# Kernel tuning notes

Measured on AMD Instinct MI355X. Metric: run time of the kernel, lower is better.

Reference implementation:

```python
import jax, jax.numpy as jnp
import numpy as np

B, S, D, T = 8, 4096, 512, 8  # batch, seq (dim), d_model, nheads


def _sinusoidal_pe(dim, d_model):
    # matches torch: pe[:,0::2]=sin(pos*div), pe[:,1::2]=cos(pos*div)
    pos = jnp.arange(dim, dtype=jnp.float32)[:, None]
    div = jnp.exp(jnp.arange(0, d_model, 2, dtype=jnp.float32) * (-(np.log(10000.0) / d_model)))
    ang = pos * div  # [dim, d_model//2]
    return jnp.stack([jnp.sin(ang), jnp.cos(ang)], axis=-1).reshape(dim, d_model)


def setup_inputs() -> dict:
    key = jax.random.key(0)
    ks = jax.random.split(key, 7)
    sc = 1.0 / np.sqrt(D)
    return {
        "x": jax.random.normal(ks[0], (B, S, D), dtype=jnp.float32),
        "Wk": jax.random.normal(ks[1], (T, D, D), dtype=jnp.float32) * sc,
        "bk": jax.random.normal(ks[2], (T, D), dtype=jnp.float32) * sc,
        "Wq": jax.random.normal(ks[3], (T, D, D), dtype=jnp.float32) * sc,
        "bq": jax.random.normal(ks[4], (T, D), dtype=jnp.float32) * sc,
        "Wv": jax.random.normal(ks[5], (T, D, D), dtype=jnp.float32) * sc,
        "bv": jax.random.normal(ks[6], (T, D), dtype=jnp.float32) * sc,
    }


def reference(x, Wk, bk, Wq, bq, Wv, bv):
    b, s, d = x.shape
    t = Wk.shape[0]
    c = s // t  # head chunk length
    x = x + _sinusoidal_pe(s, d)[None]  # PE add
    xh = x.reshape(b, t, c, d)  # 'b (t c) d -> b t c d'
    # torch Linear: y = x @ W^T + b ; W is [out, in]
    k = jnp.einsum('btcd,ted->btce', xh, Wk) + bk[None, :, None, :]
    q = jnp.einsum('btcd,ted->btce', xh, Wq) + bq[None, :, None, :]
    v = jnp.einsum('btcd,ted->btce', xh, Wv) + bv[None, :, None, :]
    # note: k @ q^T (not q @ k^T) and divide by d_model (not sqrt) -- faithful
    scores = jnp.einsum('btid,btjd->btij', k, q) * (1.0 / d)
    attn = jax.nn.softmax(scores, axis=-1)
    out = jnp.einsum('btij,btjd->btid', attn, v)
    return out.reshape(b, s, d)  # concat heads along seq dim
```

## Files before the change

kernel.cpp:

```cpp
#include <hip/hip_runtime.h>
#include <hip/hip_bf16.h>
#include <cstdint>
#include <cstddef>


typedef __bf16 bf16_t;
typedef __bf16 bf16x4 __attribute__((ext_vector_type(4)));
typedef __bf16 bf16x8 __attribute__((ext_vector_type(8)));
typedef float  f32x4  __attribute__((ext_vector_type(4)));

#define GAS __attribute__((address_space(1)))
#define LAS __attribute__((address_space(3)))

__global__ __launch_bounds__(256) void pe_cast_kernel(
    const float* __restrict__ x, bf16_t* __restrict__ xpe)
{
    const float cexp = -0.017988946039015984f;
    int i = blockIdx.x * 256 + threadIdx.x;
    int d4 = i & 127;
    int s  = i >> 7;
    int d  = d4 * 4;
    float fs = (float)s;
    float a0 = fs * __expf(cexp * (float)d);
    float a1 = fs * __expf(cexp * (float)(d + 2));
    float s0, c0, s1, c1;
    sincosf(a0, &s0, &c0);
    sincosf(a1, &s1, &c1);
    size_t base = (size_t)s * 512 + d;
    #pragma unroll
    for (int b = 0; b < 8; ++b) {
        float4 xv = *(const float4*)(x + (size_t)b * 2097152 + base);
        bf16x4 o;
        o[0] = (bf16_t)(xv.x + s0);
        o[1] = (bf16_t)(xv.y + c0);
        o[2] = (bf16_t)(xv.z + s1);
        o[3] = (bf16_t)(xv.w + c1);
        *(bf16x4*)(xpe + (size_t)b * 2097152 + base) = o;
    }
}

__global__ __launch_bounds__(256) void cast_w(
    const float* __restrict__ w0, const float* __restrict__ w1, const float* __restrict__ w2,
    bf16_t* __restrict__ o0, bf16_t* __restrict__ o1, bf16_t* __restrict__ o2, int n4)
{
    const float* s = blockIdx.y == 0 ? w0 : (blockIdx.y == 1 ? w1 : w2);
    bf16_t*      o = blockIdx.y == 0 ? o0 : (blockIdx.y == 1 ? o1 : o2);
    for (int i = blockIdx.x * 256 + threadIdx.x; i < n4; i += gridDim.x * 256) {
        float4 v = ((const float4*)s)[i];
        bf16x4 r;
        r[0] = (bf16_t)v.x; r[1] = (bf16_t)v.y; r[2] = (bf16_t)v.z; r[3] = (bf16_t)v.w;
        ((bf16x4*)o)[i] = r;
    }
}

template<int BIAS_MODE, int OUT_BF16>
__global__ __launch_bounds__(256, 2) void gemm_nt(
    const bf16_t* __restrict__ A, const bf16_t* __restrict__ Bm,
    void* __restrict__ C, const float* __restrict__ bias,
    long aStr, long bStr, long cStr, int aByT, int bByT, float scale)
{
    constexpr int LD = 512;
    int L  = blockIdx.y * 16 + blockIdx.x;
    int wk = (L & 7) * 128 + (L >> 3);
    int bt = wk >> 4;
    int tile = wk & 15;
    int t  = bt & 7;
    const bf16_t* Ab = A  + (size_t)(aByT ? t : bt) * aStr;
    const bf16_t* Bb = Bm + (size_t)(bByT ? t : bt) * bStr;
    int ti = (tile >> 2) << 7;
    int tn = (tile & 3) << 7;

    __shared__ __align__(1024) char lds[65536];

    const int tid  = threadIdx.x;
    const int l    = tid & 63;
    const int w    = tid >> 6;
    const int lrow = l >> 3;
    const int hd   = (l & 7) ^ lrow;
    const int wrow = w >> 1, wcol = w & 1;
    const int rA   = l & 15;
    const int hb   = l >> 4;
    const int x7   = l & 7;

    f32x4 acc[4][4] = {};

    auto stage = [&](int buf, int k0) {
        char* ldsA = lds + buf * 32768;
        char* ldsB = ldsA + 16384;
        #pragma unroll
        for (int p = 0; p < 4; ++p) {
            int c    = w * 4 + p;
            int grow = c * 8 + lrow;
            const bf16_t* srcA = Ab + (size_t)(ti + grow) * LD + k0 + hd * 8;
            const bf16_t* srcB = Bb + (size_t)(tn + grow) * LD + k0 + hd * 8;
            __builtin_amdgcn_global_load_lds((GAS void*)srcA, (LAS void*)(ldsA + c * 1024 + l * 16), 16, 0, 0);
            __builtin_amdgcn_global_load_lds((GAS void*)srcB, (LAS void*)(ldsB + c * 1024 + l * 16), 16, 0, 0);
        }
    };

    stage(0, 0);
    __syncthreads();
    for (int it = 0; it < 8; ++it) {
        if (it < 7) stage((it + 1) & 1, (it + 1) * 64);
        const char* ldsA = lds + (it & 1) * 32768;
        const char* ldsB = ldsA + 16384;
        #pragma unroll
        for (int kk = 0; kk < 2; ++kk) {
            bf16x8 a[4], b[4];
            #pragma unroll
            for (int m = 0; m < 4; ++m) {
                int off = (wrow * 64 + m * 16 + rA) * 128 + ((((kk << 2) | hb)) ^ x7) * 16;
                a[m] = *(const bf16x8*)(ldsA + off);
            }
            #pragma unroll
            for (int n = 0; n < 4; ++n) {
                int off = (wcol * 64 + n * 16 + rA) * 128 + ((((kk << 2) | hb)) ^ x7) * 16;
                b[n] = *(const bf16x8*)(ldsB + off);
            }
            #pragma unroll
            for (int m = 0; m < 4; ++m)
                #pragma unroll
                for (int n = 0; n < 4; ++n)
                    acc[m][n] = __builtin_amdgcn_mfma_f32_16x16x32_bf16(a[m], b[n], acc[m][n], 0, 0, 0);
        }
        __syncthreads();
    }

    const float* biasT = bias ? bias + t * 512 : bias;
    int r0 = ti + wrow * 64;
    int c0 = tn + wcol * 64;
    #pragma unroll
    for (int m = 0; m < 4; ++m) {
        #pragma unroll
        for (int n = 0; n < 4; ++n) {
            int col = c0 + n * 16 + rA;
            float bc = (BIAS_MODE == 1) ? biasT[col] : 0.0f;
            f32x4 v = acc[m][n];
            #pragma unroll
            for (int r = 0; r < 4; ++r) {
                int row = r0 + m * 16 + hb * 4 + r;
                float val = v[r] * scale + ((BIAS_MODE == 2) ? biasT[row] : bc);
                size_t off = (size_t)bt * cStr + (size_t)row * LD + col;
                if (OUT_BF16) ((bf16_t*)C)[off] = (bf16_t)val;
                else          ((float*)C)[off]  = val;
            }
        }
    }
}

__global__ __launch_bounds__(512, 2) void scores_softmax(
    const bf16_t* __restrict__ K, const bf16_t* __restrict__ Q,
    bf16_t* __restrict__ P)
{
    int L  = blockIdx.x;
    int wk = (L & 7) * 32 + (L >> 3);
    int bt = wk >> 2;
    int ti = (wk & 3) << 7;
    const bf16_t* Kb = K + (size_t)bt * 262144;
    const bf16_t* Qb = Q + (size_t)bt * 262144;

    __shared__ __align__(1024) char smem[86016];
    float* smax_p = (float*)(smem + 81920);
    float* ssum_p = (float*)(smem + 83968);

    const int tid  = threadIdx.x;
    const int l    = tid & 63;
    const int wv   = tid >> 6;
    const int wrow = wv >> 2;
    const int wcol = wv & 3;
    const int rA   = l & 15;
    const int hb   = l >> 4;

    f32x4 acc[4][8] = {};

    auto stage = [&](int buf, int d0) {
        char* kA = smem + buf * 8192;
        char* qB = smem + 16384 + buf * 32768;
        {
            int row = tid >> 2, slot = tid & 3;
            const bf16_t* src = Kb + (size_t)(ti + row) * 512 + d0 + (slot ^ (row & 3)) * 8;
            __builtin_amdgcn_global_load_lds((GAS void*)src, (LAS void*)(kA + tid * 16), 16, 0, 0);
        }
        #pragma unroll
        for (int u = 0; u < 4; ++u) {
            int q2 = u * 512 + tid;
            int row = q2 >> 2, slot = q2 & 3;
            const bf16_t* src = Qb + (size_t)row * 512 + d0 + (slot ^ (row & 3)) * 8;
            __builtin_amdgcn_global_load_lds((GAS void*)src, (LAS void*)(qB + q2 * 16), 16, 0, 0);
        }
    };

    stage(0, 0);
    __syncthreads();
    for (int it = 0; it < 16; ++it) {
        if (it < 15) stage((it + 1) & 1, (it + 1) * 32);
        const char* kA = smem + (it & 1) * 8192;
        const char* qB = smem + 16384 + (it & 1) * 32768;
        bf16x8 a[4], b[8];
        #pragma unroll
        for (int m = 0; m < 4; ++m) {
            int row = wrow * 64 + m * 16 + rA;
            a[m] = *(const bf16x8*)(kA + row * 64 + (hb ^ (row & 3)) * 16);
        }
        #pragma unroll
        for (int n = 0; n < 8; ++n) {
            int row = wcol * 128 + n * 16 + rA;
            b[n] = *(const bf16x8*)(qB + row * 64 + (hb ^ (row & 3)) * 16);
        }
        #pragma unroll
        for (int m = 0; m < 4; ++m)
            #pragma unroll
            for (int n = 0; n < 8; ++n)
                acc[m][n] = __builtin_amdgcn_mfma_f32_16x16x32_bf16(a[m], b[n], acc[m][n], 0, 0, 0);
        __syncthreads();
    }

    float red[4][4];
    #pragma unroll
    for (int m = 0; m < 4; ++m)
        #pragma unroll
        for (int r = 0; r < 4; ++r) {
            float mx = acc[m][0][r];
            #pragma unroll
            for (int n = 1; n < 8; ++n) mx = fmaxf(mx, acc[m][n][r]);
            #pragma unroll
            for (int o = 1; o < 16; o <<= 1) mx = fmaxf(mx, __shfl_xor(mx, o, 64));
            red[m][r] = mx;
        }
    if (rA < 4) {
        #pragma unroll
        for (int m = 0; m < 4; ++m)
            smax_p[(wrow * 64 + m * 16 + hb * 4 + rA) * 4 + wcol] = red[m][rA];
    }
    __syncthreads();
    float rstat[4][4];
    #pragma unroll
    for (int m = 0; m < 4; ++m)
        #pragma unroll
        for (int r = 0; r < 4; ++r) {
            f32x4 p4 = *(const f32x4*)(smax_p + (wrow * 64 + m * 16 + hb * 4 + r) * 4);
            rstat[m][r] = fmaxf(fmaxf(p4[0], p4[1]), fmaxf(p4[2], p4[3]));
        }
    const float inv512 = 1.0f / 512.0f;
    #pragma unroll
    for (int m = 0; m < 4; ++m)
        #pragma unroll
        for (int r = 0; r < 4; ++r) {
            float sum = 0.0f;
            #pragma unroll
            for (int n = 0; n < 8; ++n) {
                float e = __expf((acc[m][n][r] - rstat[m][r]) * inv512);
                acc[m][n][r] = e;
                sum += e;
            }
            #pragma unroll
            for (int o = 1; o < 16; o <<= 1) sum += __shfl_xor(sum, o, 64);
            red[m][r] = sum;
        }
    if (rA < 4) {
        #pragma unroll
        for (int m = 0; m < 4; ++m)
            ssum_p[(wrow * 64 + m * 16 + hb * 4 + rA) * 4 + wcol] = red[m][rA];
    }
    __syncthreads();
    #pragma unroll
    for (int m = 0; m < 4; ++m)
        #pragma unroll
        for (int r = 0; r < 4; ++r) {
            f32x4 p4 = *(const f32x4*)(ssum_p + (wrow * 64 + m * 16 + hb * 4 + r) * 4);
            rstat[m][r] = 1.0f / (((p4[0] + p4[1]) + (p4[2] + p4[3])));
        }
    #pragma unroll
    for (int m = 0; m < 4; ++m)
        #pragma unroll
        for (int n = 0; n < 8; ++n) {
            int col = wcol * 128 + n * 16 + rA;
            #pragma unroll
            for (int r = 0; r < 4; ++r) {
                int row = ti + wrow * 64 + m * 16 + hb * 4 + r;
                P[(size_t)bt * 262144 + (size_t)row * 512 + col] =
                    (bf16_t)(acc[m][n][r] * rstat[m][r]);
            }
        }
}

extern "C" void kernel_launch(void* const* d_in, const int* in_sizes, int n_in,
                              void* d_out, int out_size, void* d_ws, size_t ws_size,
                              hipStream_t stream)
{
    const float* x  = (const float*)d_in[0];
    const float* Wk = (const float*)d_in[1];
    const float* bk = (const float*)d_in[2];
    const float* Wq = (const float*)d_in[3];
    const float* bq = (const float*)d_in[4];
    const float* Wv = (const float*)d_in[5];
    const float* bv = (const float*)d_in[6];
    float* out = (float*)d_out;
    char*  ws  = (char*)d_ws;

    bf16_t* k    = (bf16_t*)(ws + 0);
    bf16_t* q    = (bf16_t*)(ws + 33554432);
    bf16_t* vt   = (bf16_t*)(ws + 67108864);
    bf16_t* xpe  = (bf16_t*)(ws + 100663296);
    bf16_t* attn = xpe;
    bf16_t* wkb  = (bf16_t*)(ws + 134217728);
    bf16_t* wqb  = (bf16_t*)(ws + 138412032);
    bf16_t* wvb  = (bf16_t*)(ws + 142606336);

    const long S2 = 262144;

    pe_cast_kernel<<<2048, 256, 0, stream>>>(x, xpe);
    cast_w<<<dim3(512, 3), 256, 0, stream>>>(Wk, Wq, Wv, wkb, wqb, wvb, (8 * 512 * 512) / 4);

    dim3 gg(16, 64);
    gemm_nt<1, 1><<<gg, 256, 0, stream>>>(xpe, wkb, k, bk, S2, S2, S2, 0, 1, 1.0f);
    gemm_nt<1, 1><<<gg, 256, 0, stream>>>(xpe, wqb, q, bq, S2, S2, S2, 0, 1, 1.0f);
    gemm_nt<2, 1><<<gg, 256, 0, stream>>>(wvb, xpe, vt, bv, S2, S2, S2, 1, 0, 1.0f);
    scores_softmax<<<256, 512, 0, stream>>>(k, q, attn);
    gemm_nt<0, 0><<<gg, 256, 0, stream>>>(attn, vt, out, nullptr, S2, S2, S2, 0, 0, 1.0f);
}
```

Before: 274.1 us.

## Fuse K/Q projections into one GEMM and fuse softmax with PV product

Adds a gemm_kq kernel that computes the K and Q projections together, sharing one staged tile of the PE-added input and reading both weight sets straight from global memory. The softmax kernel becomes attn_fused: it writes the normalized probabilities into swizzled LDS and multiplies them by V^T in the same block, so the bf16 attention matrix never goes to global memory and one launch is removed. The cost is more LDS per block (about 132 KB), which likely limits occupancy to one block per CU. B operands in both new kernels are loaded uncoalesced from global memory without LDS staging, which may hurt bandwidth.

```diff
diff --git a/kernel.cpp b/kernel.cpp
--- a/kernel.cpp
+++ b/kernel.cpp
@@ -53,6 +53,99 @@
     }
 }
 
+__global__ __launch_bounds__(256, 2) void gemm_kq(
+    const bf16_t* __restrict__ X, const bf16_t* __restrict__ WK,
+    const bf16_t* __restrict__ WQ, bf16_t* __restrict__ Ko,
+    bf16_t* __restrict__ Qo, const float* __restrict__ bk,
+    const float* __restrict__ bq)
+{
+    int L  = blockIdx.y * 16 + blockIdx.x;
+    int wk = (L & 7) * 128 + (L >> 3);
+    int bt = wk >> 4;
+    int tile = wk & 15;
+    int t  = bt & 7;
+    const bf16_t* Ab = X  + (size_t)bt * 262144;
+    const bf16_t* Kw = WK + (size_t)t * 262144;
+    const bf16_t* Qw = WQ + (size_t)t * 262144;
+    int ti = (tile >> 2) << 7;
+    int tn = (tile & 3) << 7;
+
+    __shared__ __align__(1024) char lds[32768];
+
+    const int tid  = threadIdx.x;
+    const int l    = tid & 63;
+    const int w    = tid >> 6;
+    const int lrow = l >> 3;
+    const int hd   = (l & 7) ^ lrow;
+    const int wrow = w >> 1, wcol = w & 1;
+    const int rA   = l & 15;
+    const int hb   = l >> 4;
+    const int x7   = l & 7;
+
+    f32x4 acck[4][4] = {}, accq[4][4] = {};
+
+    auto stage = [&](int buf, int k0) {
+        char* ldsA = lds + buf * 16384;
+        #pragma unroll
+        for (int p = 0; p < 4; ++p) {
+            int c    = w * 4 + p;
+            int grow = c * 8 + lrow;
+            const bf16_t* srcA = Ab + (size_t)(ti + grow) * 512 + k0 + hd * 8;
+            __builtin_amdgcn_global_load_lds((GAS void*)srcA, (LAS void*)(ldsA + c * 1024 + l * 16), 16, 0, 0);
+        }
+    };
+
+    stage(0, 0);
+    __syncthreads();
+    for (int it = 0; it < 8; ++it) {
+        if (it < 7) stage((it + 1) & 1, (it + 1) * 64);
+        const char* ldsA = lds + (it & 1) * 16384;
+        #pragma unroll
+        for (int kk = 0; kk < 2; ++kk) {
+            bf16x8 a[4], bK[4], bQ[4];
+            #pragma unroll
+            for (int m = 0; m < 4; ++m) {
+                int off = (wrow * 64 + m * 16 + rA) * 128 + (((kk << 2) | hb) ^ x7) * 16;
+                a[m] = *(const bf16x8*)(ldsA + off);
+            }
+            int kpos = it * 64 + kk * 32 + hb * 8;
+            #pragma unroll
+            for (int n = 0; n < 4; ++n) {
+                int e = tn + wcol * 64 + n * 16 + rA;
+                bK[n] = *(const bf16x8*)(Kw + (size_t)e * 512 + kpos);
+                bQ[n] = *(const bf16x8*)(Qw + (size_t)e * 512 + kpos);
+            }
+            #pragma unroll
+            for (int m = 0; m < 4; ++m)
+                #pragma unroll
+                for (int n = 0; n < 4; ++n) {
+                    acck[m][n] = __builtin_amdgcn_mfma_f32_16x16x32_bf16(a[m], bK[n], acck[m][n], 0, 0, 0);
+                    accq[m][n] = __builtin_amdgcn_mfma_f32_16x16x32_bf16(a[m], bQ[n], accq[m][n], 0, 0, 0);
+                }
+        }
+        __syncthreads();
+    }
+
+    const float* bkT = bk + t * 512;
+    const float* bqT = bq + t * 512;
+    int r0 = ti + wrow * 64;
+    int c0 = tn + wcol * 64;
+    #pragma unroll
+    for (int m = 0; m < 4; ++m)
+        #pragma unroll
+        for (int n = 0; n < 4; ++n) {
+            int col = c0 + n * 16 + rA;
+            float bkc = bkT[col], bqc = bqT[col];
+            #pragma unroll
+            for (int r = 0; r < 4; ++r) {
+                int row = r0 + m * 16 + hb * 4 + r;
+                size_t off = (size_t)bt * 262144 + (size_t)row * 512 + col;
+                Ko[off] = (bf16_t)(acck[m][n][r] + bkc);
+                Qo[off] = (bf16_t)(accq[m][n][r] + bqc);
+            }
+        }
+}
+
 template<int BIAS_MODE, int OUT_BF16>
 __global__ __launch_bounds__(256, 2) void gemm_nt(
     const bf16_t* __restrict__ A, const bf16_t* __restrict__ Bm,
@@ -109,12 +202,12 @@
             bf16x8 a[4], b[4];
             #pragma unroll
             for (int m = 0; m < 4; ++m) {
-                int off = (wrow * 64 + m * 16 + rA) * 128 + ((((kk << 2) | hb)) ^ x7) * 16;
+                int off = (wrow * 64 + m * 16 + rA) * 128 + (((kk << 2) | hb) ^ x7) * 16;
                 a[m] = *(const bf16x8*)(ldsA + off);
             }
             #pragma unroll
             for (int n = 0; n < 4; ++n) {
-                int off = (wcol * 64 + n * 16 + rA) * 128 + ((((kk << 2) | hb)) ^ x7) * 16;
+                int off = (wcol * 64 + n * 16 + rA) * 128 + (((kk << 2) | hb) ^ x7) * 16;
                 b[n] = *(const bf16x8*)(ldsB + off);
             }
             #pragma unroll
@@ -130,7 +223,7 @@
     int r0 = ti + wrow * 64;
     int c0 = tn + wcol * 64;
     #pragma unroll
-    for (int m = 0; m < 4; ++m) {
+    for (int m = 0; m < 4; ++m)
         #pragma unroll
         for (int n = 0; n < 4; ++n) {
             int col = c0 + n * 16 + rA;
@@ -145,23 +238,23 @@
                 else          ((float*)C)[off]  = val;
             }
         }
-    }
-}
-
-__global__ __launch_bounds__(512, 2) void scores_softmax(
+}
+
+__global__ __launch_bounds__(512, 2) void attn_fused(
     const bf16_t* __restrict__ K, const bf16_t* __restrict__ Q,
-    bf16_t* __restrict__ P)
+    const bf16_t* __restrict__ VT, float* __restrict__ Out)
 {
     int L  = blockIdx.x;
-    int wk = (L & 7) * 32 + (L >> 3);
-    int bt = wk >> 2;
-    int ti = (wk & 3) << 7;
-    const bf16_t* Kb = K + (size_t)bt * 262144;
-    const bf16_t* Qb = Q + (size_t)bt * 262144;
-
-    __shared__ __align__(1024) char smem[86016];
-    float* smax_p = (float*)(smem + 81920);
-    float* ssum_p = (float*)(smem + 83968);
+    int wkd = (L & 7) * 32 + (L >> 3);
+    int bt = wkd >> 2;
+    int ti = (wkd & 3) << 7;
+    const bf16_t* Kb = K  + (size_t)bt * 262144;
+    const bf16_t* Qb = Q  + (size_t)bt * 262144;
+    const bf16_t* Vb = VT + (size_t)bt * 262144;
+
+    __shared__ __align__(1024) char smem[135168];
+    float* smax_p = (float*)(smem + 131072);
+    float* ssum_p = (float*)(smem + 133120);
 
     const int tid  = threadIdx.x;
     const int l    = tid & 63;
@@ -268,18 +361,54 @@
         #pragma unroll
         for (int r = 0; r < 4; ++r) {
             f32x4 p4 = *(const f32x4*)(ssum_p + (wrow * 64 + m * 16 + hb * 4 + r) * 4);
-            rstat[m][r] = 1.0f / (((p4[0] + p4[1]) + (p4[2] + p4[3])));
-        }
+            rstat[m][r] = 1.0f / ((p4[0] + p4[1]) + (p4[2] + p4[3]));
+        }
+
     #pragma unroll
     for (int m = 0; m < 4; ++m)
         #pragma unroll
         for (int n = 0; n < 8; ++n) {
-            int col = wcol * 128 + n * 16 + rA;
+            int j = wcol * 128 + n * 16 + rA;
+            int jslot = j >> 3, jrem = (j & 7) * 2;
             #pragma unroll
             for (int r = 0; r < 4; ++r) {
-                int row = ti + wrow * 64 + m * 16 + hb * 4 + r;
-                P[(size_t)bt * 262144 + (size_t)row * 512 + col] =
+                int i = wrow * 64 + m * 16 + hb * 4 + r;
+                *(bf16_t*)(smem + i * 1024 + ((jslot ^ (i & 7)) << 4) + jrem) =
                     (bf16_t)(acc[m][n][r] * rstat[m][r]);
+            }
+        }
+    __syncthreads();
+
+    f32x4 acc2[4][8] = {};
+    for (int it = 0; it < 16; ++it) {
+        int j0 = it * 32;
+        bf16x8 a[4], b[8];
+        #pragma unroll
+        for (int m = 0; m < 4; ++m) {
+            int i = wrow * 64 + m * 16 + rA;
+            a[m] = *(const bf16x8*)(smem + i * 1024 + ((((it << 2) | hb) ^ (i & 7)) << 4));
+        }
+        #pragma unroll
+        for (int n = 0; n < 8; ++n) {
+            int e = wcol * 128 + n * 16 + rA;
+            b[n] = *(const bf16x8*)(Vb + (size_t)e * 512 + j0 + hb * 8);
+        }
+        #pragma unroll
+        for (int m = 0; m < 4; ++m)
+            #pragma unroll
+            for (int n = 0; n < 8; ++n)
+                acc2[m][n] = __builtin_amdgcn_mfma_f32_16x16x32_bf16(a[m], b[n], acc2[m][n], 0, 0, 0);
+    }
+
+    #pragma unroll
+    for (int m = 0; m < 4; ++m)
+        #pragma unroll
+        for (int n = 0; n < 8; ++n) {
+            int e = wcol * 128 + n * 16 + rA;
+            #pragma unroll
+            for (int r = 0; r < 4; ++r) {
+                int i = ti + wrow * 64 + m * 16 + hb * 4 + r;
+                Out[(size_t)bt * 262144 + (size_t)i * 512 + e] = acc2[m][n][r];
             }
         }
 }
@@ -302,7 +431,6 @@
     bf16_t* q    = (bf16_t*)(ws + 33554432);
     bf16_t* vt   = (bf16_t*)(ws + 67108864);
     bf16_t* xpe  = (bf16_t*)(ws + 100663296);
-    bf16_t* attn = xpe;
     bf16_t* wkb  = (bf16_t*)(ws + 134217728);
     bf16_t* wqb  = (bf16_t*)(ws + 138412032);
     bf16_t* wvb  = (bf16_t*)(ws + 142606336);
@@ -313,9 +441,7 @@
     cast_w<<<dim3(512, 3), 256, 0, stream>>>(Wk, Wq, Wv, wkb, wqb, wvb, (8 * 512 * 512) / 4);
 
     dim3 gg(16, 64);
-    gemm_nt<1, 1><<<gg, 256, 0, stream>>>(xpe, wkb, k, bk, S2, S2, S2, 0, 1, 1.0f);
-    gemm_nt<1, 1><<<gg, 256, 0, stream>>>(xpe, wqb, q, bq, S2, S2, S2, 0, 1, 1.0f);
+    gemm_kq<<<gg, 256, 0, stream>>>(xpe, wkb, wqb, k, q, bk, bq);
     gemm_nt<2, 1><<<gg, 256, 0, stream>>>(wvb, xpe, vt, bv, S2, S2, S2, 1, 0, 1.0f);
-    scores_softmax<<<256, 512, 0, stream>>>(k, q, attn);
-    gemm_nt<0, 0><<<gg, 256, 0, stream>>>(attn, vt, out, nullptr, S2, S2, S2, 0, 0, 1.0f);
-}
+    attn_fused<<<256, 512, 0, stream>>>(k, q, vt, out);
+}
```

After: 327.3 us. +19.4%, slower.

## Fuse scores-softmax with PV matmul and merge prep kernels

Applied to the files above, without the earlier changes.

Replaces the separate scores/softmax kernel and the final P@V GEMM with a single attention kernel. Each block handles 64 query rows, keeps the normalized probabilities in swizzled LDS and streams V^T tiles to produce the fp32 output directly, so the bf16 attention matrix is never written to or re-read from global memory. The PE-add cast and the weight cast are merged into one launch, and the GEMM block-to-tile mapping is reordered to group heads. The fused kernel uses about 140KB of LDS, which limits it to one block per CU, and the K/Q tiles are smaller per block.

```diff
diff --git a/kernel.cpp b/kernel.cpp
--- a/kernel.cpp
+++ b/kernel.cpp
@@ -12,44 +12,48 @@
 #define GAS __attribute__((address_space(1)))
 #define LAS __attribute__((address_space(3)))
 
-__global__ __launch_bounds__(256) void pe_cast_kernel(
-    const float* __restrict__ x, bf16_t* __restrict__ xpe)
+__global__ __launch_bounds__(256) void prep_kernel(
+    const float* __restrict__ x, bf16_t* __restrict__ xpe,
+    const float* __restrict__ w0, const float* __restrict__ w1,
+    const float* __restrict__ w2, bf16_t* __restrict__ o0,
+    bf16_t* __restrict__ o1, bf16_t* __restrict__ o2)
 {
-    const float cexp = -0.017988946039015984f;
-    int i = blockIdx.x * 256 + threadIdx.x;
-    int d4 = i & 127;
-    int s  = i >> 7;
-    int d  = d4 * 4;
-    float fs = (float)s;
-    float a0 = fs * __expf(cexp * (float)d);
-    float a1 = fs * __expf(cexp * (float)(d + 2));
-    float s0, c0, s1, c1;
-    sincosf(a0, &s0, &c0);
-    sincosf(a1, &s1, &c1);
-    size_t base = (size_t)s * 512 + d;
-    #pragma unroll
-    for (int b = 0; b < 8; ++b) {
-        float4 xv = *(const float4*)(x + (size_t)b * 2097152 + base);
-        bf16x4 o;
-        o[0] = (bf16_t)(xv.x + s0);
-        o[1] = (bf16_t)(xv.y + c0);
-        o[2] = (bf16_t)(xv.z + s1);
-        o[3] = (bf16_t)(xv.w + c1);
-        *(bf16x4*)(xpe + (size_t)b * 2097152 + base) = o;
-    }
-}
-
-__global__ __launch_bounds__(256) void cast_w(
-    const float* __restrict__ w0, const float* __restrict__ w1, const float* __restrict__ w2,
-    bf16_t* __restrict__ o0, bf16_t* __restrict__ o1, bf16_t* __restrict__ o2, int n4)
-{
-    const float* s = blockIdx.y == 0 ? w0 : (blockIdx.y == 1 ? w1 : w2);
-    bf16_t*      o = blockIdx.y == 0 ? o0 : (blockIdx.y == 1 ? o1 : o2);
-    for (int i = blockIdx.x * 256 + threadIdx.x; i < n4; i += gridDim.x * 256) {
-        float4 v = ((const float4*)s)[i];
-        bf16x4 r;
-        r[0] = (bf16_t)v.x; r[1] = (bf16_t)v.y; r[2] = (bf16_t)v.z; r[3] = (bf16_t)v.w;
-        ((bf16x4*)o)[i] = r;
+    if (blockIdx.x < 2048) {
+        const float cexp = -0.017988946039015984f;
+        int i = blockIdx.x * 256 + threadIdx.x;
+        int d4 = i & 127;
+        int s  = i >> 7;
+        int d  = d4 * 4;
+        float fs = (float)s;
+        float a0 = fs * __expf(cexp * (float)d);
+        float a1 = fs * __expf(cexp * (float)(d + 2));
+        float s0, c0, s1, c1;
+        sincosf(a0, &s0, &c0);
+        sincosf(a1, &s1, &c1);
+        size_t base = (size_t)s * 512 + d;
+        #pragma unroll
+        for (int b = 0; b < 8; ++b) {
+            float4 xv = *(const float4*)(x + (size_t)b * 2097152 + base);
+            bf16x4 o;
+            o[0] = (bf16_t)(xv.x + s0);
+            o[1] = (bf16_t)(xv.y + c0);
+            o[2] = (bf16_t)(xv.z + s1);
+            o[3] = (bf16_t)(xv.w + c1);
+            *(bf16x4*)(xpe + (size_t)b * 2097152 + base) = o;
+        }
+    } else {
+        const int per = 524288;
+        for (int i = (blockIdx.x - 2048) * 256 + threadIdx.x; i < 3 * per;
+             i += 1024 * 256) {
+            int f = i / per, off = i - f * per;
+            const float* s = f == 0 ? w0 : (f == 1 ? w1 : w2);
+            bf16_t*      o = f == 0 ? o0 : (f == 1 ? o1 : o2);
+            float4 v = ((const float4*)s)[off];
+            bf16x4 r;
+            r[0] = (bf16_t)v.x; r[1] = (bf16_t)v.y;
+            r[2] = (bf16_t)v.z; r[3] = (bf16_t)v.w;
+            ((bf16x4*)o)[off] = r;
+        }
     }
 }
 
@@ -61,10 +65,10 @@
 {
     constexpr int LD = 512;
     int L  = blockIdx.y * 16 + blockIdx.x;
-    int wk = (L & 7) * 128 + (L >> 3);
-    int bt = wk >> 4;
-    int tile = wk & 15;
-    int t  = bt & 7;
+    int t  = L & 7;
+    int b  = (L >> 3) & 7;
+    int tile = L >> 6;
+    int bt = (b << 3) | t;
     const bf16_t* Ab = A  + (size_t)(aByT ? t : bt) * aStr;
     const bf16_t* Bb = Bm + (size_t)(bByT ? t : bt) * bStr;
     int ti = (tile >> 2) << 7;
@@ -106,22 +110,22 @@
         const char* ldsB = ldsA + 16384;
         #pragma unroll
         for (int kk = 0; kk < 2; ++kk) {
-            bf16x8 a[4], b[4];
+            bf16x8 a[4], bb[4];
             #pragma unroll
             for (int m = 0; m < 4; ++m) {
-                int off = (wrow * 64 + m * 16 + rA) * 128 + ((((kk << 2) | hb)) ^ x7) * 16;
+                int off = (wrow * 64 + m * 16 + rA) * 128 + (((kk << 2) | hb) ^ x7) * 16;
                 a[m] = *(const bf16x8*)(ldsA + off);
             }
             #pragma unroll
             for (int n = 0; n < 4; ++n) {
-                int off = (wcol * 64 + n * 16 + rA) * 128 + ((((kk << 2) | hb)) ^ x7) * 16;
-                b[n] = *(const bf16x8*)(ldsB + off);
+                int off = (wcol * 64 + n * 16 + rA) * 128 + (((kk << 2) | hb) ^ x7) * 16;
+                bb[n] = *(const bf16x8*)(ldsB + off);
             }
             #pragma unroll
             for (int m = 0; m < 4; ++m)
                 #pragma unroll
                 for (int n = 0; n < 4; ++n)
-                    acc[m][n] = __builtin_amdgcn_mfma_f32_16x16x32_bf16(a[m], b[n], acc[m][n], 0, 0, 0);
+                    acc[m][n] = __builtin_amdgcn_mfma_f32_16x16x32_bf16(a[m], bb[n], acc[m][n], 0, 0, 0);
         }
         __syncthreads();
     }
@@ -130,7 +134,7 @@
     int r0 = ti + wrow * 64;
     int c0 = tn + wcol * 64;
     #pragma unroll
-    for (int m = 0; m < 4; ++m) {
+    for (int m = 0; m < 4; ++m)
         #pragma unroll
         for (int n = 0; n < 4; ++n) {
             int col = c0 + n * 16 + rA;
@@ -145,72 +149,73 @@
                 else          ((float*)C)[off]  = val;
             }
         }
-    }
 }
 
-__global__ __launch_bounds__(512, 2) void scores_softmax(
+__global__ __launch_bounds__(512) void attn_fused(
     const bf16_t* __restrict__ K, const bf16_t* __restrict__ Q,
-    bf16_t* __restrict__ P)
+    const bf16_t* __restrict__ VT, float* __restrict__ Out)
 {
     int L  = blockIdx.x;
-    int wk = (L & 7) * 32 + (L >> 3);
-    int bt = wk >> 2;
-    int ti = (wk & 3) << 7;
-    const bf16_t* Kb = K + (size_t)bt * 262144;
-    const bf16_t* Qb = Q + (size_t)bt * 262144;
-
-    __shared__ __align__(1024) char smem[86016];
-    float* smax_p = (float*)(smem + 81920);
-    float* ssum_p = (float*)(smem + 83968);
-
-    const int tid  = threadIdx.x;
-    const int l    = tid & 63;
-    const int wv   = tid >> 6;
-    const int wrow = wv >> 2;
-    const int wcol = wv & 3;
-    const int rA   = l & 15;
-    const int hb   = l >> 4;
-
-    f32x4 acc[4][8] = {};
-
-    auto stage = [&](int buf, int d0) {
-        char* kA = smem + buf * 8192;
-        char* qB = smem + 16384 + buf * 32768;
-        {
-            int row = tid >> 2, slot = tid & 3;
-            const bf16_t* src = Kb + (size_t)(ti + row) * 512 + d0 + (slot ^ (row & 3)) * 8;
+    int bt = ((L >> 6) << 3) | (L & 7);
+    int ti = ((L >> 3) & 7) << 6;
+    const bf16_t* Kb = K  + (size_t)bt * 262144;
+    const bf16_t* Qb = Q  + (size_t)bt * 262144;
+    const bf16_t* Vb = VT + (size_t)bt * 262144;
+
+    __shared__ __align__(1024) char smem[143360];
+    char* Pl = smem + 73728;
+    float* smax_p = (float*)(smem + 139264);
+    float* ssum_p = (float*)(smem + 141312);
+
+    const int tid = threadIdx.x;
+    const int l   = tid & 63;
+    const int wv  = tid >> 6;
+    const int rA  = l & 15;
+    const int hb  = l >> 4;
+    const int key = (rA >> 1) & 3;
+
+    const int srow = tid >> 2;
+    const int sslot = tid & 3;
+
+    f32x4 acc[4][4] = {};
+
+    auto stageKQ = [&](int buf, int d0) {
+        char* kA = smem + buf * 4096;
+        char* qB = smem + 8192 + buf * 32768;
+        if (tid < 256) {
+            const bf16_t* src = Kb + (size_t)(ti + srow) * 512 + d0 +
+                                (sslot ^ ((srow >> 1) & 3)) * 8;
             __builtin_amdgcn_global_load_lds((GAS void*)src, (LAS void*)(kA + tid * 16), 16, 0, 0);
         }
         #pragma unroll
         for (int u = 0; u < 4; ++u) {
             int q2 = u * 512 + tid;
             int row = q2 >> 2, slot = q2 & 3;
-            const bf16_t* src = Qb + (size_t)row * 512 + d0 + (slot ^ (row & 3)) * 8;
+            const bf16_t* src = Qb + (size_t)row * 512 + d0 +
+                                (slot ^ ((row >> 1) & 3)) * 8;
             __builtin_amdgcn_global_load_lds((GAS void*)src, (LAS void*)(qB + q2 * 16), 16, 0, 0);
         }
     };
 
-    stage(0, 0);
+    stageKQ(0, 0);
     __syncthreads();
     for (int it = 0; it < 16; ++it) {
-        if (it < 15) stage((it + 1) & 1, (it + 1) * 32);
-        const char* kA = smem + (it & 1) * 8192;
-        const char* qB = smem + 16384 + (it & 1) * 32768;
-        bf16x8 a[4], b[8];
-        #pragma unroll
-        for (int m = 0; m < 4; ++m) {
-            int row = wrow * 64 + m * 16 + rA;
-            a[m] = *(const bf16x8*)(kA + row * 64 + (hb ^ (row & 3)) * 16);
-        }
-        #pragma unroll
-        for (int n = 0; n < 8; ++n) {
-            int row = wcol * 128 + n * 16 + rA;
-            b[n] = *(const bf16x8*)(qB + row * 64 + (hb ^ (row & 3)) * 16);
-        }
-        #pragma unroll
-        for (int m = 0; m < 4; ++m)
-            #pragma unroll
-            for (int n = 0; n < 8; ++n)
+        if (it < 15) stageKQ((it + 1) & 1, (it + 1) * 32);
+        const char* kA = smem + (it & 1) * 4096;
+        const char* qB = smem + 8192 + (it & 1) * 32768;
+        bf16x8 a[4], b[4];
+        #pragma unroll
+        for (int m = 0; m < 4; ++m)
+            a[m] = *(const bf16x8*)(kA + (m * 16 + rA) * 64 + ((hb ^ key) << 4));
+        #pragma unroll
+        for (int n = 0; n < 4; ++n) {
+            int j = wv * 64 + n * 16 + rA;
+            b[n] = *(const bf16x8*)(qB + j * 64 + ((hb ^ key) << 4));
+        }
+        #pragma unroll
+        for (int m = 0; m < 4; ++m)
+            #pragma unroll
+            for (int n = 0; n < 4; ++n)
                 acc[m][n] = __builtin_amdgcn_mfma_f32_16x16x32_bf16(a[m], b[n], acc[m][n], 0, 0, 0);
         __syncthreads();
     }
@@ -222,7 +227,7 @@
         for (int r = 0; r < 4; ++r) {
             float mx = acc[m][0][r];
             #pragma unroll
-            for (int n = 1; n < 8; ++n) mx = fmaxf(mx, acc[m][n][r]);
+            for (int n = 1; n < 4; ++n) mx = fmaxf(mx, acc[m][n][r]);
             #pragma unroll
             for (int o = 1; o < 16; o <<= 1) mx = fmaxf(mx, __shfl_xor(mx, o, 64));
             red[m][r] = mx;
@@ -230,7 +235,7 @@
     if (rA < 4) {
         #pragma unroll
         for (int m = 0; m < 4; ++m)
-            smax_p[(wrow * 64 + m * 16 + hb * 4 + rA) * 4 + wcol] = red[m][rA];
+            smax_p[(m * 16 + hb * 4 + rA) * 8 + wv] = red[m][rA];
     }
     __syncthreads();
     float rstat[4][4];
@@ -238,8 +243,11 @@
     for (int m = 0; m < 4; ++m)
         #pragma unroll
         for (int r = 0; r < 4; ++r) {
-            f32x4 p4 = *(const f32x4*)(smax_p + (wrow * 64 + m * 16 + hb * 4 + r) * 4);
-            rstat[m][r] = fmaxf(fmaxf(p4[0], p4[1]), fmaxf(p4[2], p4[3]));
+            int row = m * 16 + hb * 4 + r;
+            f32x4 p0 = *(const f32x4*)(smax_p + row * 8);
+            f32x4 p1 = *(const f32x4*)(smax_p + row * 8 + 4);
+            rstat[m][r] = fmaxf(fmaxf(fmaxf(p0[0], p0[1]), fmaxf(p0[2], p0[3])),
+                                fmaxf(fmaxf(p1[0], p1[1]), fmaxf(p1[2], p1[3])));
         }
     const float inv512 = 1.0f / 512.0f;
     #pragma unroll
@@ -248,7 +256,7 @@
         for (int r = 0; r < 4; ++r) {
             float sum = 0.0f;
             #pragma unroll
-            for (int n = 0; n < 8; ++n) {
+            for (int n = 0; n < 4; ++n) {
                 float e = __expf((acc[m][n][r] - rstat[m][r]) * inv512);
                 acc[m][n][r] = e;
                 sum += e;
@@ -260,26 +268,82 @@
     if (rA < 4) {
         #pragma unroll
         for (int m = 0; m < 4; ++m)
-            ssum_p[(wrow * 64 + m * 16 + hb * 4 + rA) * 4 + wcol] = red[m][rA];
+            ssum_p[(m * 16 + hb * 4 + rA) * 8 + wv] = red[m][rA];
     }
     __syncthreads();
     #pragma unroll
     for (int m = 0; m < 4; ++m)
         #pragma unroll
         for (int r = 0; r < 4; ++r) {
-            f32x4 p4 = *(const f32x4*)(ssum_p + (wrow * 64 + m * 16 + hb * 4 + r) * 4);
-            rstat[m][r] = 1.0f / (((p4[0] + p4[1]) + (p4[2] + p4[3])));
-        }
-    #pragma unroll
-    for (int m = 0; m < 4; ++m)
-        #pragma unroll
-        for (int n = 0; n < 8; ++n) {
-            int col = wcol * 128 + n * 16 + rA;
+            int row = m * 16 + hb * 4 + r;
+            f32x4 p0 = *(const f32x4*)(ssum_p + row * 8);
+            f32x4 p1 = *(const f32x4*)(ssum_p + row * 8 + 4);
+            rstat[m][r] = 1.0f / (((p0[0] + p0[1]) + (p0[2] + p0[3])) +
+                                  ((p1[0] + p1[1]) + (p1[2] + p1[3])));
+        }
+
+    #pragma unroll
+    for (int m = 0; m < 4; ++m)
+        #pragma unroll
+        for (int n = 0; n < 4; ++n) {
+            int j = wv * 64 + n * 16 + rA;
+            int jslot = j >> 3, jrem = (j & 7) * 2;
             #pragma unroll
             for (int r = 0; r < 4; ++r) {
-                int row = ti + wrow * 64 + m * 16 + hb * 4 + r;
-                P[(size_t)bt * 262144 + (size_t)row * 512 + col] =
+                int i = m * 16 + hb * 4 + r;
+                *(bf16_t*)(Pl + i * 1024 + ((jslot ^ (i & 7)) << 4) + jrem) =
                     (bf16_t)(acc[m][n][r] * rstat[m][r]);
+            }
+        }
+    __syncthreads();
+
+    auto stageV = [&](int buf, int j0) {
+        char* vB = smem + 8192 + buf * 32768;
+        #pragma unroll
+        for (int u = 0; u < 4; ++u) {
+            int q2 = u * 512 + tid;
+            int e = q2 >> 2, slot = q2 & 3;
+            const bf16_t* src = Vb + (size_t)e * 512 + j0 +
+                                (slot ^ ((e >> 1) & 3)) * 8;
+            __builtin_amdgcn_global_load_lds((GAS void*)src, (LAS void*)(vB + q2 * 16), 16, 0, 0);
+        }
+    };
+
+    f32x4 acc2[4][4] = {};
+    stageV(0, 0);
+    __syncthreads();
+    for (int it = 0; it < 16; ++it) {
+        if (it < 15) stageV((it + 1) & 1, (it + 1) * 32);
+        const char* vB = smem + 8192 + (it & 1) * 32768;
+        int jcb = it * 4;
+        bf16x8 a[4], b[4];
+        #pragma unroll
+        for (int m = 0; m < 4; ++m) {
+            int i = m * 16 + rA;
+            a[m] = *(const bf16x8*)(Pl + i * 1024 + (((jcb + hb) ^ (i & 7)) << 4));
+        }
+        #pragma unroll
+        for (int n = 0; n < 4; ++n) {
+            int e = wv * 64 + n * 16 + rA;
+            b[n] = *(const bf16x8*)(vB + e * 64 + ((hb ^ key) << 4));
+        }
+        #pragma unroll
+        for (int m = 0; m < 4; ++m)
+            #pragma unroll
+            for (int n = 0; n < 4; ++n)
+                acc2[m][n] = __builtin_amdgcn_mfma_f32_16x16x32_bf16(a[m], b[n], acc2[m][n], 0, 0, 0);
+        __syncthreads();
+    }
+
+    #pragma unroll
+    for (int m = 0; m < 4; ++m)
+        #pragma unroll
+        for (int n = 0; n < 4; ++n) {
+            int e = wv * 64 + n * 16 + rA;
+            #pragma unroll
+            for (int r = 0; r < 4; ++r) {
+                int i = ti + m * 16 + hb * 4 + r;
+                Out[(size_t)bt * 262144 + (size_t)i * 512 + e] = acc2[m][n][r];
             }
         }
 }
@@ -302,20 +366,17 @@
     bf16_t* q    = (bf16_t*)(ws + 33554432);
     bf16_t* vt   = (bf16_t*)(ws + 67108864);
     bf16_t* xpe  = (bf16_t*)(ws + 100663296);
-    bf16_t* attn = xpe;
     bf16_t* wkb  = (bf16_t*)(ws + 134217728);
     bf16_t* wqb  = (bf16_t*)(ws + 138412032);
     bf16_t* wvb  = (bf16_t*)(ws + 142606336);
 
     const long S2 = 262144;
 
-    pe_cast_kernel<<<2048, 256, 0, stream>>>(x, xpe);
-    cast_w<<<dim3(512, 3), 256, 0, stream>>>(Wk, Wq, Wv, wkb, wqb, wvb, (8 * 512 * 512) / 4);
+    prep_kernel<<<3072, 256, 0, stream>>>(x, xpe, Wk, Wq, Wv, wkb, wqb, wvb);
 
     dim3 gg(16, 64);
     gemm_nt<1, 1><<<gg, 256, 0, stream>>>(xpe, wkb, k, bk, S2, S2, S2, 0, 1, 1.0f);
     gemm_nt<1, 1><<<gg, 256, 0, stream>>>(xpe, wqb, q, bq, S2, S2, S2, 0, 1, 1.0f);
     gemm_nt<2, 1><<<gg, 256, 0, stream>>>(wvb, xpe, vt, bv, S2, S2, S2, 1, 0, 1.0f);
-    scores_softmax<<<256, 512, 0, stream>>>(k, q, attn);
-    gemm_nt<0, 0><<<gg, 256, 0, stream>>>(attn, vt, out, nullptr, S2, S2, S2, 0, 0, 1.0f);
+    attn_fused<<<512, 512, 0, stream>>>(k, q, vt, out);
 }
```

After: 284.7 us. +3.9%, slower.
